# Performance work log

Measured on AMD Instinct MI355X. Metric: run time of the kernel, lower is better.

Reference implementation:

```python
import jax, jax.numpy as jnp
import numpy as np


def ray_sampler(cam2world, intrinsics, resolution):
    # EG3D RaySampler: pixel centers in [0,1], lifted through intrinsics, rotated to world.
    B = cam2world.shape[0]
    fx = intrinsics[:, 0, 0][:, None]
    fy = intrinsics[:, 1, 1][:, None]
    cx = intrinsics[:, 0, 2][:, None]
    cy = intrinsics[:, 1, 2][:, None]
    sk = intrinsics[:, 0, 1][:, None]
    ii, jj = jnp.meshgrid(jnp.arange(resolution), jnp.arange(resolution), indexing='ij')
    # torch.meshgrid + flip(0): x = column index, y = row index (row-major flatten)
    x = ((jj.reshape(-1).astype(jnp.float32) + 0.5) / resolution)[None, :]  # [1, M]
    y = ((ii.reshape(-1).astype(jnp.float32) + 0.5) / resolution)[None, :]  # [1, M]
    x_lift = (x - cx + cy * sk / fy - sk * y / fy) / fx        # [B, M]
    y_lift = (y - cy) / fy                                     # [B, M]
    ones = jnp.ones_like(x_lift)
    cam_rel = jnp.stack([x_lift, y_lift, ones, ones], axis=-1)  # [B, M, 4]
    world = jnp.einsum('bij,bmj->bmi', cam2world, cam_rel)[..., :3]  # [B, M, 3]
    cam_loc = cam2world[:, :3, 3]                               # [B, 3]
    dirs = world - cam_loc[:, None, :]
    dirs = dirs / jnp.maximum(jnp.linalg.norm(dirs, axis=-1, keepdims=True), 1e-12)
    origins = jnp.broadcast_to(cam_loc[:, None, :], dirs.shape)
    return origins, dirs


def setup_inputs() -> dict:
    key = jax.random.key(0)
    k1, k2, k3 = jax.random.split(key, 3)
    B, res, N = 4, 128, 2048
    # realistic camera: identity rotation, camera near z=2.7 (EG3D radius), normalized intrinsics
    t = jnp.concatenate([0.05 * jax.random.normal(k1, (B, 2)), jnp.full((B, 1), 2.7)], axis=1)
    c2w = jnp.tile(jnp.eye(4, dtype=jnp.float32)[None], (B, 1, 1)).at[:, :3, 3].set(t)
    intr = jnp.tile(jnp.array([[4.2647, 0.0, 0.5], [0.0, 4.2647, 0.5], [0.0, 0.0, 1.0]],
                              dtype=jnp.float32)[None], (B, 1, 1))
    c = jnp.concatenate([c2w.reshape(B, 16), intr.reshape(B, 9)], axis=1)  # [B, 25]
    image_depth = 2.2 + jax.random.uniform(k2, (B, 1, res, res), dtype=jnp.float32)
    pc = 0.3 * jax.random.normal(k3, (B, N, 3), dtype=jnp.float32)
    return {"c": c, "image_depth": image_depth, "pc": pc, "neural_rendering_resolution": 128}


def reference(c, image_depth, pc, neural_rendering_resolution):
    B = c.shape[0]
    res = neural_rendering_resolution
    M = res * res
    cam2world = c[:, :16].reshape(B, 4, 4)
    intrinsics = c[:, 16:25].reshape(B, 3, 3)
    ray_origins, ray_dirs = ray_sampler(cam2world, intrinsics, res)  # [B, M, 3] each
    pc3 = pc[..., :3]                                                # [B, N, 3]
    # distance from camera origin to every pc point -> max per sample
    d0 = jnp.linalg.norm(ray_origins[:, :1, :] - pc3, axis=-1)       # [B, N]
    max_distance = jnp.max(d0, axis=1)                               # [B]
    depth = image_depth.reshape(B, M, 1)
    pred = depth * ray_dirs + ray_origins                            # [B, M, 3]
    mask = depth.reshape(B, M) < max_distance[:, None]               # [B, M]
    # chamfer dist1 (direction=0): squared distance of each pred point to nearest pc point
    d2 = (jnp.sum(pred * pred, axis=-1)[:, :, None]
          + jnp.sum(pc3 * pc3, axis=-1)[:, None, :]
          - 2.0 * jnp.einsum('bmd,bnd->bmn', pred, pc3))             # [B, M, N]
    min_d2 = jnp.maximum(jnp.min(d2, axis=2), 0.0)                   # [B, M]
    # ragged masked mean == mean over pred_[mask_] in the original loop
    m = mask.astype(min_d2.dtype)
    loss = jnp.sum(min_d2 * m, axis=1) / jnp.maximum(jnp.sum(m, axis=1), 1.0)
    return loss.reshape(B, 1)
```

## Files before the change

kernel.cpp:

```cpp
#include <hip/hip_runtime.h>
#include <math.h>

#define WAVES 8
#define TPB 512
#define RPT 4
#define RAYS_PB 256
#define MAXPTS 2048

__global__ __launch_bounds__(256) void prep_kernel(
    const float* __restrict__ c, const float* __restrict__ pc,
    float4* __restrict__ pts4, float* __restrict__ maxdist, int N)
{
    int b = blockIdx.x;
    const float* cb = c + b * 25;
    float ox = cb[3], oy = cb[7], oz = cb[11];
    const float* p = pc + (size_t)b * N * 3;
    float mx = -3.4e38f;
    for (int n = threadIdx.x; n < N; n += blockDim.x) {
        float qx = p[n * 3 + 0], qy = p[n * 3 + 1], qz = p[n * 3 + 2];
        float qn = qx * qx + qy * qy + qz * qz;
        pts4[(size_t)b * N + n] = make_float4(qx, qy, qz, -0.5f * qn);
        float dx = qx - ox, dy = qy - oy, dz = qz - oz;
        mx = fmaxf(mx, dx * dx + dy * dy + dz * dz);
    }
    for (int off = 32; off; off >>= 1) mx = fmaxf(mx, __shfl_down(mx, off));
    __shared__ float sred[8];
    int wid = threadIdx.x >> 6;
    if ((threadIdx.x & 63) == 0) sred[wid] = mx;
    __syncthreads();
    if (threadIdx.x == 0) {
        float m2 = sred[0];
        int nw = blockDim.x >> 6;
        for (int w = 1; w < nw; ++w) m2 = fmaxf(m2, sred[w]);
        maxdist[b] = sqrtf(m2);
    }
}

__global__ __launch_bounds__(TPB) void chamfer_kernel(
    const float* __restrict__ c, const float* __restrict__ depth,
    const float4* __restrict__ pts4, const float* __restrict__ maxdist,
    float2* __restrict__ partial, int res, int M, int N)
{
    __shared__ float4 spts[MAXPTS];
    __shared__ float red[WAVES][RAYS_PB];
    __shared__ float bs[WAVES], bc[WAVES];

    int b = blockIdx.z;
    int r0 = blockIdx.x * RAYS_PB;
    int tid = threadIdx.x;
    int w = tid >> 6, lane = tid & 63;

    const float* cb = c + b * 25;
    float fx = cb[16], sk = cb[17], cx = cb[18];
    float fy = cb[20], cy = cb[21];
    float ox = cb[3], oy = cb[7], oz = cb[11];

    float px[RPT], py[RPT], pz[RPT], pn[RPT], dep[RPT], mxs[RPT];
    #pragma unroll
    for (int r = 0; r < RPT; ++r) {
        int m = r0 + lane + 64 * r;
        int mm = min(m, M - 1);
        int i = mm / res, j = mm - i * res;
        float x = (j + 0.5f) / (float)res;
        float y = (i + 0.5f) / (float)res;
        float xl = (x - cx + cy * sk / fy - sk * y / fy) / fx;
        float yl = (y - cy) / fy;
        float wx = cb[0] * xl + cb[1] * yl + cb[2] + cb[3];
        float wy = cb[4] * xl + cb[5] * yl + cb[6] + cb[7];
        float wz = cb[8] * xl + cb[9] * yl + cb[10] + cb[11];
        float dx = wx - ox, dy = wy - oy, dz = wz - oz;
        float nrm = fmaxf(sqrtf(dx * dx + dy * dy + dz * dz), 1e-12f);
        dx /= nrm; dy /= nrm; dz /= nrm;
        float d = depth[(size_t)b * M + mm];
        dep[r] = d;
        px[r] = fmaf(d, dx, ox);
        py[r] = fmaf(d, dy, oy);
        pz[r] = fmaf(d, dz, oz);
        pn[r] = px[r] * px[r] + py[r] * py[r] + pz[r] * pz[r];
        mxs[r] = -3.4e38f;
    }

    for (int n0 = 0; n0 < N; n0 += MAXPTS) {
        int nend = min(N - n0, MAXPTS);
        __syncthreads();
        const float4* src = pts4 + (size_t)b * N + n0;
        for (int k2 = tid; k2 < nend; k2 += TPB) spts[k2] = src[k2];
        __syncthreads();
        int cpw = (nend + WAVES - 1) / WAVES;
        int ks = min(w * cpw, nend);
        int kc = min(nend - ks, cpw);
        const float4* sp = spts + ks;
        #pragma unroll 8
        for (int k = 0; k < kc; ++k) {
            float4 q = sp[k];
            #pragma unroll
            for (int r = 0; r < RPT; ++r) {
                float s = fmaf(px[r], q.x, q.w);
                s = fmaf(py[r], q.y, s);
                s = fmaf(pz[r], q.z, s);
                mxs[r] = fmaxf(mxs[r], s);
            }
        }
    }

    #pragma unroll
    for (int r = 0; r < RPT; ++r) red[w][lane + 64 * r] = mxs[r];
    __syncthreads();

    float s = 0.f, cnt = 0.f;
    if (tid < RAYS_PB) {
        float mx = red[0][tid];
        #pragma unroll
        for (int ww = 1; ww < WAVES; ++ww) mx = fmaxf(mx, red[ww][tid]);
        int k = tid >> 6;
        float pnk = pn[0], dk = dep[0];
        #pragma unroll
        for (int r = 1; r < RPT; ++r) if (k == r) { pnk = pn[r]; dk = dep[r]; }
        int m = r0 + tid;
        if (m < M) {
            float md = fmaxf(fmaf(2.0f, mx, pnk), 0.0f);
            md = fmaxf(fmaf(-2.0f, mx, pnk), 0.0f);
            if (dk < maxdist[b]) { s = md; cnt = 1.0f; }
        }
    }
    for (int off = 32; off; off >>= 1) {
        s += __shfl_down(s, off);
        cnt += __shfl_down(cnt, off);
    }
    if (lane == 0) { bs[w] = s; bc[w] = cnt; }
    __syncthreads();
    if (tid == 0) {
        float S = 0.f, C = 0.f;
        #pragma unroll
        for (int ww = 0; ww < WAVES; ++ww) { S += bs[ww]; C += bc[ww]; }
        partial[(size_t)b * gridDim.x + blockIdx.x] = make_float2(S, C);
    }
}

__global__ __launch_bounds__(64) void finalize_kernel(
    const float2* __restrict__ partial, float* __restrict__ out, int nblk)
{
    int b = blockIdx.x;
    float S = 0.f, C = 0.f;
    for (int i = threadIdx.x; i < nblk; i += 64) {
        float2 p = partial[(size_t)b * nblk + i];
        S += p.x; C += p.y;
    }
    for (int off = 32; off; off >>= 1) {
        S += __shfl_down(S, off);
        C += __shfl_down(C, off);
    }
    if (threadIdx.x == 0) out[b] = S / fmaxf(C, 1.0f);
}

extern "C" void kernel_launch(void* const* d_in, const int* in_sizes, int n_in,
                              void* d_out, int out_size, void* d_ws, size_t ws_size,
                              hipStream_t stream) {
    const float* c     = (const float*)d_in[0];
    const float* depth = (const float*)d_in[1];
    const float* pc    = (const float*)d_in[2];

    int B = in_sizes[0] / 25;
    int M = in_sizes[1] / B;
    int N = in_sizes[2] / (3 * B);
    int res = 1;
    while (res * res < M) ++res;

    char* base = (char*)d_ws;
    float4* pts4 = (float4*)base;
    size_t off_maxdist = (size_t)B * N * sizeof(float4);
    float* maxdist = (float*)(base + off_maxdist);
    float2* partial = (float2*)(base + off_maxdist + 256);

    int nblk = (M + RAYS_PB - 1) / RAYS_PB;

    prep_kernel<<<B, 256, 0, stream>>>(c, pc, pts4, maxdist, N);

    dim3 grid(nblk, 1, B);
    chamfer_kernel<<<grid, TPB, 0, stream>>>(c, depth, pts4, maxdist, partial,
                                             res, M, N);

    finalize_kernel<<<B, 64, 0, stream>>>(partial, (float*)d_out, nblk);
}
```

Before: 25.91 us.

## Fuse point prep into chamfer kernel and split point set across two blocks

```diff
diff --git a/kernel.cpp b/kernel.cpp
--- a/kernel.cpp
+++ b/kernel.cpp
@@ -1,64 +1,38 @@
 #include <hip/hip_runtime.h>
 #include <math.h>
 
+#define TPB 512
 #define WAVES 8
-#define TPB 512
-#define RPT 4
-#define RAYS_PB 256
-#define MAXPTS 2048
+#define RAYS_PB 512
+#define RPT 8
+#define MAXK 1024
 
-__global__ __launch_bounds__(256) void prep_kernel(
-    const float* __restrict__ c, const float* __restrict__ pc,
-    float4* __restrict__ pts4, float* __restrict__ maxdist, int N)
+__global__ __launch_bounds__(TPB) void chamfer_main(
+    const float* __restrict__ c, const float* __restrict__ depth,
+    const float* __restrict__ pc,
+    float* __restrict__ partmax,
+    float* __restrict__ pnbuf,
+    float* __restrict__ gmaxd,
+    int res, int M, int N, int K)
 {
-    int b = blockIdx.x;
-    const float* cb = c + b * 25;
-    float ox = cb[3], oy = cb[7], oz = cb[11];
-    const float* p = pc + (size_t)b * N * 3;
-    float mx = -3.4e38f;
-    for (int n = threadIdx.x; n < N; n += blockDim.x) {
-        float qx = p[n * 3 + 0], qy = p[n * 3 + 1], qz = p[n * 3 + 2];
-        float qn = qx * qx + qy * qy + qz * qz;
-        pts4[(size_t)b * N + n] = make_float4(qx, qy, qz, -0.5f * qn);
-        float dx = qx - ox, dy = qy - oy, dz = qz - oz;
-        mx = fmaxf(mx, dx * dx + dy * dy + dz * dz);
-    }
-    for (int off = 32; off; off >>= 1) mx = fmaxf(mx, __shfl_down(mx, off));
-    __shared__ float sred[8];
-    int wid = threadIdx.x >> 6;
-    if ((threadIdx.x & 63) == 0) sred[wid] = mx;
-    __syncthreads();
-    if (threadIdx.x == 0) {
-        float m2 = sred[0];
-        int nw = blockDim.x >> 6;
-        for (int w = 1; w < nw; ++w) m2 = fmaxf(m2, sred[w]);
-        maxdist[b] = sqrtf(m2);
-    }
-}
+    __shared__ float4 spts[MAXK];
+    __shared__ float red[WAVES][RAYS_PB];
+    __shared__ float smax[WAVES];
 
-__global__ __launch_bounds__(TPB) void chamfer_kernel(
-    const float* __restrict__ c, const float* __restrict__ depth,
-    const float4* __restrict__ pts4, const float* __restrict__ maxdist,
-    float2* __restrict__ partial, int res, int M, int N)
-{
-    __shared__ float4 spts[MAXPTS];
-    __shared__ float red[WAVES][RAYS_PB];
-    __shared__ float bs[WAVES], bc[WAVES];
-
+    int tile = blockIdx.x;
+    int h = blockIdx.y;
     int b = blockIdx.z;
-    int r0 = blockIdx.x * RAYS_PB;
-    int tid = threadIdx.x;
-    int w = tid >> 6, lane = tid & 63;
+    int tid = threadIdx.x, w = tid >> 6, lane = tid & 63;
 
     const float* cb = c + b * 25;
     float fx = cb[16], sk = cb[17], cx = cb[18];
     float fy = cb[20], cy = cb[21];
     float ox = cb[3], oy = cb[7], oz = cb[11];
 
-    float px[RPT], py[RPT], pz[RPT], pn[RPT], dep[RPT], mxs[RPT];
+    float px[RPT], py[RPT], pz[RPT], pn[RPT], mxs[RPT];
     #pragma unroll
     for (int r = 0; r < RPT; ++r) {
-        int m = r0 + lane + 64 * r;
+        int m = tile * RAYS_PB + lane + 64 * r;
         int mm = min(m, M - 1);
         int i = mm / res, j = mm - i * res;
         float x = (j + 0.5f) / (float)res;
@@ -72,7 +46,6 @@
         float nrm = fmaxf(sqrtf(dx * dx + dy * dy + dz * dz), 1e-12f);
         dx /= nrm; dy /= nrm; dz /= nrm;
         float d = depth[(size_t)b * M + mm];
-        dep[r] = d;
         px[r] = fmaf(d, dx, ox);
         py[r] = fmaf(d, dy, oy);
         pz[r] = fmaf(d, dz, oz);
@@ -80,77 +53,100 @@
         mxs[r] = -3.4e38f;
     }
 
-    for (int n0 = 0; n0 < N; n0 += MAXPTS) {
-        int nend = min(N - n0, MAXPTS);
+    int ks = h * K;
+    int khalf = max(0, min(N - ks, K));
+    float mdl = -3.4e38f;
+    float* raw = (float*)red;
+
+    for (int c0 = 0; c0 < khalf; c0 += MAXK) {
+        int kc = min(khalf - c0, MAXK);
         __syncthreads();
-        const float4* src = pts4 + (size_t)b * N + n0;
-        for (int k2 = tid; k2 < nend; k2 += TPB) spts[k2] = src[k2];
+        const float* src = pc + ((size_t)b * N + ks + c0) * 3;
+        int nf = kc * 3;
+        for (int i2 = tid; i2 < nf; i2 += TPB) raw[i2] = src[i2];
         __syncthreads();
-        int cpw = (nend + WAVES - 1) / WAVES;
-        int ks = min(w * cpw, nend);
-        int kc = min(nend - ks, cpw);
-        const float4* sp = spts + ks;
-        #pragma unroll 8
-        for (int k = 0; k < kc; ++k) {
-            float4 q = sp[k];
+        for (int p = tid; p < kc; p += TPB) {
+            float qx = raw[3 * p], qy = raw[3 * p + 1], qz = raw[3 * p + 2];
+            float qn = qx * qx + qy * qy + qz * qz;
+            spts[p] = make_float4(qx, qy, qz, -0.5f * qn);
+            float dx = qx - ox, dy = qy - oy, dz = qz - oz;
+            mdl = fmaxf(mdl, dx * dx + dy * dy + dz * dz);
+        }
+        __syncthreads();
+
+        int cpw = (kc + WAVES - 1) / WAVES;
+        int s0 = min(w * cpw, kc);
+        int s1 = min(s0 + cpw, kc);
+        #pragma unroll 2
+        for (int k = s0; k < s1; ++k) {
+            float4 q = spts[k];
             #pragma unroll
             for (int r = 0; r < RPT; ++r) {
-                float s = fmaf(px[r], q.x, q.w);
+                float s = fmaf(pz[r], q.z, q.w);
                 s = fmaf(py[r], q.y, s);
-                s = fmaf(pz[r], q.z, s);
+                s = fmaf(px[r], q.x, s);
                 mxs[r] = fmaxf(mxs[r], s);
             }
         }
     }
 
+    for (int off = 32; off; off >>= 1) mdl = fmaxf(mdl, __shfl_down(mdl, off));
+    if (lane == 0) smax[w] = mdl;
+
+    __syncthreads();
     #pragma unroll
     for (int r = 0; r < RPT; ++r) red[w][lane + 64 * r] = mxs[r];
     __syncthreads();
 
-    float s = 0.f, cnt = 0.f;
-    if (tid < RAYS_PB) {
+    {
         float mx = red[0][tid];
         #pragma unroll
         for (int ww = 1; ww < WAVES; ++ww) mx = fmaxf(mx, red[ww][tid]);
-        int k = tid >> 6;
-        float pnk = pn[0], dk = dep[0];
+        float pnk = pn[0];
         #pragma unroll
-        for (int r = 1; r < RPT; ++r) if (k == r) { pnk = pn[r]; dk = dep[r]; }
-        int m = r0 + tid;
+        for (int r = 1; r < RPT; ++r) if (w == r) pnk = pn[r];
+        int m = tile * RAYS_PB + tid;
         if (m < M) {
-            float md = fmaxf(fmaf(2.0f, mx, pnk), 0.0f);
-            md = fmaxf(fmaf(-2.0f, mx, pnk), 0.0f);
-            if (dk < maxdist[b]) { s = md; cnt = 1.0f; }
+            partmax[((size_t)(b * 2 + h)) * M + m] = mx;
+            if (h == 0) pnbuf[(size_t)b * M + m] = pnk;
         }
+    }
+    if (tid == 0) {
+        float m2 = smax[0];
+        #pragma unroll
+        for (int ww = 1; ww < WAVES; ++ww) m2 = fmaxf(m2, smax[ww]);
+        gmaxd[b * 2 + h] = sqrtf(fmaxf(m2, 0.0f));
+    }
+}
+
+__global__ __launch_bounds__(1024) void chamfer_finalize(
+    const float* __restrict__ partmax, const float* __restrict__ pnbuf,
+    const float* __restrict__ gmaxd, const float* __restrict__ depth,
+    float* __restrict__ out, int M)
+{
+    int b = blockIdx.x;
+    float thr = fmaxf(gmaxd[2 * b], gmaxd[2 * b + 1]);
+    float s = 0.f, cnt = 0.f;
+    for (int m = threadIdx.x; m < M; m += 1024) {
+        float mx = fmaxf(partmax[(size_t)(2 * b) * M + m],
+                         partmax[(size_t)(2 * b + 1) * M + m]);
+        float md = fmaxf(fmaf(-2.0f, mx, pnbuf[(size_t)b * M + m]), 0.0f);
+        if (depth[(size_t)b * M + m] < thr) { s += md; cnt += 1.0f; }
     }
     for (int off = 32; off; off >>= 1) {
         s += __shfl_down(s, off);
         cnt += __shfl_down(cnt, off);
     }
-    if (lane == 0) { bs[w] = s; bc[w] = cnt; }
+    __shared__ float ss[16], sc[16];
+    int w = threadIdx.x >> 6;
+    if ((threadIdx.x & 63) == 0) { ss[w] = s; sc[w] = cnt; }
     __syncthreads();
-    if (tid == 0) {
+    if (threadIdx.x == 0) {
         float S = 0.f, C = 0.f;
         #pragma unroll
-        for (int ww = 0; ww < WAVES; ++ww) { S += bs[ww]; C += bc[ww]; }
-        partial[(size_t)b * gridDim.x + blockIdx.x] = make_float2(S, C);
+        for (int ww = 0; ww < 16; ++ww) { S += ss[ww]; C += sc[ww]; }
+        out[b] = S / fmaxf(C, 1.0f);
     }
-}
-
-__global__ __launch_bounds__(64) void finalize_kernel(
-    const float2* __restrict__ partial, float* __restrict__ out, int nblk)
-{
-    int b = blockIdx.x;
-    float S = 0.f, C = 0.f;
-    for (int i = threadIdx.x; i < nblk; i += 64) {
-        float2 p = partial[(size_t)b * nblk + i];
-        S += p.x; C += p.y;
-    }
-    for (int off = 32; off; off >>= 1) {
-        S += __shfl_down(S, off);
-        C += __shfl_down(C, off);
-    }
-    if (threadIdx.x == 0) out[b] = S / fmaxf(C, 1.0f);
 }
 
 extern "C" void kernel_launch(void* const* d_in, const int* in_sizes, int n_in,
@@ -166,19 +162,20 @@
     int res = 1;
     while (res * res < M) ++res;
 
+    int K = (N + 1) / 2;
+
     char* base = (char*)d_ws;
-    float4* pts4 = (float4*)base;
-    size_t off_maxdist = (size_t)B * N * sizeof(float4);
-    float* maxdist = (float*)(base + off_maxdist);
-    float2* partial = (float2*)(base + off_maxdist + 256);
+    float* partmax = (float*)base;
+    size_t o1 = (size_t)B * 2 * M * sizeof(float);
+    float* pnbuf = (float*)(base + o1);
+    size_t o2 = o1 + (size_t)B * M * sizeof(float);
+    o2 = (o2 + 255) & ~(size_t)255;
+    float* gmaxd = (float*)(base + o2);
 
-    int nblk = (M + RAYS_PB - 1) / RAYS_PB;
-
-    prep_kernel<<<B, 256, 0, stream>>>(c, pc, pts4, maxdist, N);
-
-    dim3 grid(nblk, 1, B);
-    chamfer_kernel<<<grid, TPB, 0, stream>>>(c, depth, pts4, maxdist, partial,
-                                             res, M, N);
-
-    finalize_kernel<<<B, 64, 0, stream>>>(partial, (float*)d_out, nblk);
+    int ntiles = (M + RAYS_PB - 1) / RAYS_PB;
+    dim3 grid(ntiles, 2, B);
+    chamfer_main<<<grid, TPB, 0, stream>>>(c, depth, pc, partmax, pnbuf, gmaxd,
+                                           res, M, N, K);
+    chamfer_finalize<<<B, 1024, 0, stream>>>(partmax, pnbuf, gmaxd, depth,
+                                             (float*)d_out, M);
 }
```

New measurement: 30.01 us. +15.8%, slower.

## Parallelize prep across blocks and read points directly from global in chamfer loop

Applied to the files above, without the earlier changes.

```diff
diff --git a/kernel.cpp b/kernel.cpp
--- a/kernel.cpp
+++ b/kernel.cpp
@@ -1,64 +1,68 @@
 #include <hip/hip_runtime.h>
 #include <math.h>
 
+#define TPB 512
 #define WAVES 8
-#define TPB 512
+#define RAYS_PB 256
 #define RPT 4
-#define RAYS_PB 256
-#define MAXPTS 2048
+#define PREP_BLK 16
+#define PREP_T 128
 
-__global__ __launch_bounds__(256) void prep_kernel(
+__global__ __launch_bounds__(PREP_T) void prep_kernel(
     const float* __restrict__ c, const float* __restrict__ pc,
-    float4* __restrict__ pts4, float* __restrict__ maxdist, int N)
+    float4* __restrict__ pts4, float* __restrict__ gpart, int N)
 {
-    int b = blockIdx.x;
+    int b = blockIdx.y, blk = blockIdx.x;
     const float* cb = c + b * 25;
     float ox = cb[3], oy = cb[7], oz = cb[11];
     const float* p = pc + (size_t)b * N * 3;
-    float mx = -3.4e38f;
-    for (int n = threadIdx.x; n < N; n += blockDim.x) {
-        float qx = p[n * 3 + 0], qy = p[n * 3 + 1], qz = p[n * 3 + 2];
+    int per = (N + PREP_BLK - 1) / PREP_BLK;
+    int n0 = blk * per;
+    int n1 = min(n0 + per, N);
+    float mx = 0.0f;
+    for (int n = n0 + threadIdx.x; n < n1; n += PREP_T) {
+        float qx = p[n * 3], qy = p[n * 3 + 1], qz = p[n * 3 + 2];
         float qn = qx * qx + qy * qy + qz * qz;
         pts4[(size_t)b * N + n] = make_float4(qx, qy, qz, -0.5f * qn);
         float dx = qx - ox, dy = qy - oy, dz = qz - oz;
         mx = fmaxf(mx, dx * dx + dy * dy + dz * dz);
     }
     for (int off = 32; off; off >>= 1) mx = fmaxf(mx, __shfl_down(mx, off));
-    __shared__ float sred[8];
-    int wid = threadIdx.x >> 6;
-    if ((threadIdx.x & 63) == 0) sred[wid] = mx;
+    __shared__ float sm[PREP_T / 64];
+    if ((threadIdx.x & 63) == 0) sm[threadIdx.x >> 6] = mx;
     __syncthreads();
     if (threadIdx.x == 0) {
-        float m2 = sred[0];
-        int nw = blockDim.x >> 6;
-        for (int w = 1; w < nw; ++w) m2 = fmaxf(m2, sred[w]);
-        maxdist[b] = sqrtf(m2);
+        float m2 = sm[0];
+        for (int i = 1; i < PREP_T / 64; ++i) m2 = fmaxf(m2, sm[i]);
+        gpart[b * PREP_BLK + blk] = m2;
     }
 }
 
-__global__ __launch_bounds__(TPB) void chamfer_kernel(
+__global__ __launch_bounds__(TPB) void chamfer_main(
     const float* __restrict__ c, const float* __restrict__ depth,
-    const float4* __restrict__ pts4, const float* __restrict__ maxdist,
+    const float4* __restrict__ pts4, const float* __restrict__ gpart,
     float2* __restrict__ partial, int res, int M, int N)
 {
-    __shared__ float4 spts[MAXPTS];
     __shared__ float red[WAVES][RAYS_PB];
-    __shared__ float bs[WAVES], bc[WAVES];
+    __shared__ float bs[RPT], bc[RPT];
 
-    int b = blockIdx.z;
-    int r0 = blockIdx.x * RAYS_PB;
-    int tid = threadIdx.x;
-    int w = tid >> 6, lane = tid & 63;
+    int tile = blockIdx.x, b = blockIdx.y;
+    int tid = threadIdx.x, w = tid >> 6, lane = tid & 63;
 
     const float* cb = c + b * 25;
     float fx = cb[16], sk = cb[17], cx = cb[18];
     float fy = cb[20], cy = cb[21];
     float ox = cb[3], oy = cb[7], oz = cb[11];
 
+    float m2 = 0.0f;
+    #pragma unroll
+    for (int i = 0; i < PREP_BLK; ++i) m2 = fmaxf(m2, gpart[b * PREP_BLK + i]);
+    float thr = sqrtf(m2);
+
     float px[RPT], py[RPT], pz[RPT], pn[RPT], dep[RPT], mxs[RPT];
     #pragma unroll
     for (int r = 0; r < RPT; ++r) {
-        int m = r0 + lane + 64 * r;
+        int m = tile * RAYS_PB + lane + 64 * r;
         int mm = min(m, M - 1);
         int i = mm / res, j = mm - i * res;
         float x = (j + 0.5f) / (float)res;
@@ -80,24 +84,19 @@
         mxs[r] = -3.4e38f;
     }
 
-    for (int n0 = 0; n0 < N; n0 += MAXPTS) {
-        int nend = min(N - n0, MAXPTS);
-        __syncthreads();
-        const float4* src = pts4 + (size_t)b * N + n0;
-        for (int k2 = tid; k2 < nend; k2 += TPB) spts[k2] = src[k2];
-        __syncthreads();
-        int cpw = (nend + WAVES - 1) / WAVES;
-        int ks = min(w * cpw, nend);
-        int kc = min(nend - ks, cpw);
-        const float4* sp = spts + ks;
-        #pragma unroll 8
-        for (int k = 0; k < kc; ++k) {
-            float4 q = sp[k];
+    {
+        int cpw = (N + WAVES - 1) / WAVES;
+        int s0 = min(w * cpw, N);
+        int s1 = min(s0 + cpw, N);
+        const float4* pq = pts4 + (size_t)b * N;
+        #pragma unroll 4
+        for (int k = s0; k < s1; ++k) {
+            float4 q = pq[k];
             #pragma unroll
             for (int r = 0; r < RPT; ++r) {
-                float s = fmaf(px[r], q.x, q.w);
+                float s = fmaf(pz[r], q.z, q.w);
                 s = fmaf(py[r], q.y, s);
-                s = fmaf(pz[r], q.z, s);
+                s = fmaf(px[r], q.x, s);
                 mxs[r] = fmaxf(mxs[r], s);
             }
         }
@@ -112,27 +111,25 @@
         float mx = red[0][tid];
         #pragma unroll
         for (int ww = 1; ww < WAVES; ++ww) mx = fmaxf(mx, red[ww][tid]);
-        int k = tid >> 6;
         float pnk = pn[0], dk = dep[0];
         #pragma unroll
-        for (int r = 1; r < RPT; ++r) if (k == r) { pnk = pn[r]; dk = dep[r]; }
-        int m = r0 + tid;
+        for (int r = 1; r < RPT; ++r) if (w == r) { pnk = pn[r]; dk = dep[r]; }
+        int m = tile * RAYS_PB + tid;
         if (m < M) {
-            float md = fmaxf(fmaf(2.0f, mx, pnk), 0.0f);
-            md = fmaxf(fmaf(-2.0f, mx, pnk), 0.0f);
-            if (dk < maxdist[b]) { s = md; cnt = 1.0f; }
+            float md = fmaxf(fmaf(-2.0f, mx, pnk), 0.0f);
+            if (dk < thr) { s = md; cnt = 1.0f; }
         }
     }
     for (int off = 32; off; off >>= 1) {
         s += __shfl_down(s, off);
         cnt += __shfl_down(cnt, off);
     }
-    if (lane == 0) { bs[w] = s; bc[w] = cnt; }
+    if (tid < RAYS_PB && lane == 0) { bs[w] = s; bc[w] = cnt; }
     __syncthreads();
     if (tid == 0) {
         float S = 0.f, C = 0.f;
         #pragma unroll
-        for (int ww = 0; ww < WAVES; ++ww) { S += bs[ww]; C += bc[ww]; }
+        for (int ww = 0; ww < RPT; ++ww) { S += bs[ww]; C += bc[ww]; }
         partial[(size_t)b * gridDim.x + blockIdx.x] = make_float2(S, C);
     }
 }
@@ -168,17 +165,17 @@
 
     char* base = (char*)d_ws;
     float4* pts4 = (float4*)base;
-    size_t off_maxdist = (size_t)B * N * sizeof(float4);
-    float* maxdist = (float*)(base + off_maxdist);
-    float2* partial = (float2*)(base + off_maxdist + 256);
+    size_t o1 = (size_t)B * N * sizeof(float4);
+    o1 = (o1 + 255) & ~(size_t)255;
+    float* gpart = (float*)(base + o1);
+    size_t o2 = o1 + (size_t)B * PREP_BLK * sizeof(float);
+    o2 = (o2 + 255) & ~(size_t)255;
+    float2* partial = (float2*)(base + o2);
 
-    int nblk = (M + RAYS_PB - 1) / RAYS_PB;
+    int ntiles = (M + RAYS_PB - 1) / RAYS_PB;
 
-    prep_kernel<<<B, 256, 0, stream>>>(c, pc, pts4, maxdist, N);
-
-    dim3 grid(nblk, 1, B);
-    chamfer_kernel<<<grid, TPB, 0, stream>>>(c, depth, pts4, maxdist, partial,
-                                             res, M, N);
-
-    finalize_kernel<<<B, 64, 0, stream>>>(partial, (float*)d_out, nblk);
+    prep_kernel<<<dim3(PREP_BLK, B), PREP_T, 0, stream>>>(c, pc, pts4, gpart, N);
+    chamfer_main<<<dim3(ntiles, B), TPB, 0, stream>>>(c, depth, pts4, gpart,
+                                                      partial, res, M, N);
+    finalize_kernel<<<B, 64, 0, stream>>>(partial, (float*)d_out, ntiles);
 }
```

Measured after the change: 35.86 us. 38.4% more time.
